# Performance work log

Hardware: AMD Instinct MI355X
Metric: run time of the kernel (lower is better)

## Reference

```python
import jax, jax.numpy as jnp
import numpy as np

T, B, D_IN, D_H = 512, 256, 128, 128


def setup_inputs() -> dict:
    key = jax.random.key(0)
    ks = jax.random.split(key, 13)
    D = D_IN + D_H
    s = 1.0 / np.sqrt(D)  # torch nn.Linear default init bound
    inp = {"inputs": jax.random.normal(ks[0], (T, B, D_IN), jnp.float32)}
    for i, n in enumerate(["forget", "input", "update", "output"]):
        inp[f"W_{n}"] = jax.random.uniform(ks[1 + 3 * i], (2, D), jnp.float32, -s, s)
        inp[f"b_{n}"] = jax.random.uniform(ks[2 + 3 * i], (2,), jnp.float32, -s, s)
        inp[f"theta_{n}"] = jax.random.uniform(ks[3 + 3 * i], (2,), jnp.float32, 0.0, 2.0 * np.pi)
    return inp


def _qgate(comb, W, b, theta):
    # SamplerQNN analytic form (2 qubits):
    #   RY(x0)RY(th0) on wire0, RY(x1)RY(th1) on wire1, CNOT(0,1), measure <Z0>.
    #   Consecutive RYs compose; Z0 commutes with CNOT (wire0 is control),
    #   so QLayer output = <Z0> = cos(x0 + th0). Wire-1 params do not affect it.
    z0 = comb @ W[0] + b[0]  # first row of the 2-dim Linear projection: (B,)
    return jnp.cos(z0 + theta[0])


def reference(inputs, W_forget, b_forget, theta_forget, W_input, b_input, theta_input,
              W_update, b_update, theta_update, W_output, b_output, theta_output):
    Bsz = inputs.shape[1]
    h0 = jnp.zeros((Bsz, D_H), inputs.dtype)
    c0 = jnp.zeros((Bsz, D_H), inputs.dtype)

    def step(carry, x_t):
        hx, cx = carry
        comb = jnp.concatenate([x_t, hx], axis=1)  # (B, D_IN + D_H)
        # per-batch scalar gate activations, broadcast over hidden dim
        f = jax.nn.sigmoid(_qgate(comb, W_forget, b_forget, theta_forget))[:, None]
        i = jax.nn.sigmoid(_qgate(comb, W_input, b_input, theta_input))[:, None]
        g = jnp.tanh(_qgate(comb, W_update, b_update, theta_update))[:, None]
        o = jax.nn.sigmoid(_qgate(comb, W_output, b_output, theta_output))[:, None]
        cx = f * cx + i * g
        hx = o * jnp.tanh(cx)
        return (hx, cx), hx

    (hx, cx), outputs = jax.lax.scan(step, (h0, c0), inputs)
    return outputs, hx, cx
```

## Files before the change

### kernel.cpp

```cpp
#include <hip/hip_runtime.h>
#include <hip/hip_bf16.h>


constexpr int T = 512;
constexpr int Bsz = 256;
constexpr int R = T * Bsz;
constexpr float INV2PI = 0.15915494309189535f;

__global__ __launch_bounds__(256) void xz_kernel(
    const float* __restrict__ x,
    const float* __restrict__ Wf, const float* __restrict__ bf, const float* __restrict__ tf,
    const float* __restrict__ Wi, const float* __restrict__ bi, const float* __restrict__ ti,
    const float* __restrict__ Wu, const float* __restrict__ bu, const float* __restrict__ tu,
    const float* __restrict__ Wo, const float* __restrict__ bo, const float* __restrict__ to_,
    float4* __restrict__ xz)
{
    const int wglobal = blockIdx.x * 4 + (threadIdx.x >> 6);
    const int lane = threadIdx.x & 63;
    const int hl = lane & 31;
    const int half = lane >> 5;

    const float4 wfv = ((const float4*)Wf)[hl];
    const float4 wiv = ((const float4*)Wi)[hl];
    const float4 wuv = ((const float4*)Wu)[hl];
    const float4 wov = ((const float4*)Wo)[hl];

    const float cf = bf[0] + tf[0];
    const float ci = bi[0] + ti[0];
    const float cu = bu[0] + tu[0];
    const float co = bo[0] + to_[0];

    for (int it = 0; it < 8; ++it) {
        const int row = (it * 8192 + wglobal) * 2 + half;
        const float4 xv = *(const float4*)(x + (size_t)row * 128 + hl * 4);

        float pf = xv.x * wfv.x + xv.y * wfv.y + xv.z * wfv.z + xv.w * wfv.w;
        float pi = xv.x * wiv.x + xv.y * wiv.y + xv.z * wiv.z + xv.w * wiv.w;
        float pu = xv.x * wuv.x + xv.y * wuv.y + xv.z * wuv.z + xv.w * wuv.w;
        float po = xv.x * wov.x + xv.y * wov.y + xv.z * wov.z + xv.w * wov.w;

#pragma unroll
        for (int off = 16; off; off >>= 1) {
            pf += __shfl_xor(pf, off, 64);
            pi += __shfl_xor(pi, off, 64);
            pu += __shfl_xor(pu, off, 64);
            po += __shfl_xor(po, off, 64);
        }
        if (hl == 0) {
            xz[row] = make_float4((pf + cf) * INV2PI, (pi + ci) * INV2PI,
                                  (pu + cu) * INV2PI, (po + co) * INV2PI);
        }
    }
}

__device__ __forceinline__ float tanh9(float c) {
    const float y  = c * c;
    const float y2 = y * y;
    const float lo  = fmaf(y, -0.321470f, 0.999168f);
    const float hi  = fmaf(y, 0.0016407f, -0.0199491f);
    const float mid = fmaf(y, hi, 0.101498f);
    return c * fmaf(y2, mid, lo);
}

template<int CTRL>
__device__ __forceinline__ float dppq(float x) {
    return __builtin_bit_cast(float,
        __builtin_amdgcn_mov_dpp(__builtin_bit_cast(int, x), CTRL, 0xF, 0xF, true));
}

__device__ __forceinline__ float wsum(const float* __restrict__ W, int lane) {
    float s = W[128 + lane] + W[192 + lane];
#pragma unroll
    for (int off = 32; off; off >>= 1) s += __shfl_xor(s, off, 64);
    return s;
}

constexpr int BPB = 8;
constexpr int SCAN_BLOCKS = Bsz / BPB;

__global__ __launch_bounds__(256, 1) void scan_kernel(
    const float4* __restrict__ xz,
    const float* __restrict__ Wf, const float* __restrict__ Wi,
    const float* __restrict__ Wu, const float* __restrict__ Wo,
    float* __restrict__ hscan, float* __restrict__ cfin)
{
    __shared__ float4 lds4[T * BPB];
    const int tid = threadIdx.x;
    const int bb = blockIdx.x * BPB;

#pragma unroll
    for (int k = 0; k < T * BPB / 256; ++k) {
        const int j = k * 256 + tid;
        lds4[j] = xz[(j >> 3) * Bsz + bb + (j & 7)];
    }

    const int l = tid & 63;
    const float swf = wsum(Wf, l) * INV2PI;
    const float swi = wsum(Wi, l) * INV2PI;
    const float swu = wsum(Wu, l) * INV2PI;
    const float swo = wsum(Wo, l) * INV2PI;

    __syncthreads();
    if (tid >= BPB * 4) return;

    const int q = tid & 3;
    const int bg = tid >> 2;
    const int batch = bb + bg;

    const float sw = (q == 0) ? swf : (q == 1) ? swi : (q == 2) ? swu : swo;

    const bool tq = (q == 2);
    const float K0 = tq ? 0.0f        : 0.5f;
    const float K1 = tq ? 0.999904f   : 0.249976f;
    const float K3 = tq ? -0.331066f  : -0.0206916f;
    const float K5 = tq ? 0.120476f   : 0.00188244f;
    const float K7 = tq ? -0.0277200f : -0.000108281f;

    const float* zl = (const float*)lds4 + tid;
    float* hp = hscan + batch;

    float h = 0.0f, c = 0.0f;

#define QSTEP(Z)                                                  \
    {                                                             \
        const float u  = fmaf(h, sw, (Z));                        \
        const float v  = __builtin_amdgcn_cosf(u);                \
        const float v2 = v * v;                                   \
        const float v4 = v2 * v2;                                 \
        const float ph = fmaf(v2, K7, K5);                        \
        const float pl = fmaf(v2, K3, K1);                        \
        const float gown = fmaf(v, fmaf(v4, ph, pl), K0);         \
        const float f = dppq<0x00>(gown);                         \
        const float i = dppq<0x55>(gown);                         \
        const float g = dppq<0xAA>(gown);                         \
        const float o = dppq<0xFF>(gown);                         \
        c = fmaf(f, c, i * g);                                    \
        h = o * tanh9(c);                                         \
        *hp = h;                                                  \
        hp += Bsz;                                                \
    }

    for (int tb = 0; tb < T; tb += 8) {
        const float* zt = zl + (size_t)tb * 32;
        const float y0 = zt[0 * 32];
        const float y1 = zt[1 * 32];
        const float y2 = zt[2 * 32];
        const float y3 = zt[3 * 32];
        const float y4 = zt[4 * 32];
        const float y5 = zt[5 * 32];
        const float y6 = zt[6 * 32];
        const float y7 = zt[7 * 32];
        QSTEP(y0); QSTEP(y1); QSTEP(y2); QSTEP(y3);
        QSTEP(y4); QSTEP(y5); QSTEP(y6); QSTEP(y7);
    }
#undef QSTEP

    cfin[batch] = c;
}

__global__ __launch_bounds__(256) void bcast_kernel(
    const float* __restrict__ hscan, const float* __restrict__ cfin,
    float4* __restrict__ out)
{
    const unsigned i = blockIdx.x * 256u + threadIdx.x;
    const unsigned row = i >> 5;
    float v;
    if (row < (unsigned)R) {
        v = hscan[row];
    } else {
        const unsigned r2 = row - (unsigned)R;
        v = (r2 < (unsigned)Bsz) ? hscan[(T - 1) * Bsz + r2] : cfin[r2 - (unsigned)Bsz];
    }
    out[i] = make_float4(v, v, v, v);
}

extern "C" void kernel_launch(void* const* d_in, const int* in_sizes, int n_in,
                              void* d_out, int out_size, void* d_ws, size_t ws_size,
                              hipStream_t stream)
{
    const float* x  = (const float*)d_in[0];
    const float* Wf = (const float*)d_in[1];
    const float* bf = (const float*)d_in[2];
    const float* tf = (const float*)d_in[3];
    const float* Wi = (const float*)d_in[4];
    const float* bi = (const float*)d_in[5];
    const float* ti = (const float*)d_in[6];
    const float* Wu = (const float*)d_in[7];
    const float* bu = (const float*)d_in[8];
    const float* tu = (const float*)d_in[9];
    const float* Wo = (const float*)d_in[10];
    const float* bo = (const float*)d_in[11];
    const float* to_ = (const float*)d_in[12];

    float* ws    = (float*)d_ws;
    float4* xz   = (float4*)ws;
    float* hscan = ws + 4 * R;
    float* cfin  = ws + 5 * R;

    xz_kernel<<<2048, 256, 0, stream>>>(x, Wf, bf, tf, Wi, bi, ti, Wu, bu, tu, Wo, bo, to_, xz);
    scan_kernel<<<SCAN_BLOCKS, 256, 0, stream>>>(xz, Wf, Wi, Wu, Wo, hscan, cfin);

    const int total_f4 = (R + 2 * Bsz) * 32;
    bcast_kernel<<<total_f4 / 256, 256, 0, stream>>>(hscan, cfin, (float4*)d_out);
}
```

Baseline: 73.80 us.

## Buffer scan hidden states in LDS and flush coalesced; shorten gate polynomial

The serial scan loop now writes each step's h into a shared-memory buffer rather than issuing a scattered global store every step. After the loop, all 256 threads copy the buffer to hscan with coalesced stores. The gate activation polynomial is also cut from degree 7 to degree 5 with refitted tanh constants, which removes a few FMAs from the serial critical path. The trade-offs are extra LDS (a 64KB buffer on top of the z buffer), slightly lower accuracy of the gate activation, and an added barrier plus a copy phase at the end of the kernel.

```diff
diff --git a/kernel.cpp b/kernel.cpp
--- a/kernel.cpp
+++ b/kernel.cpp
@@ -84,14 +84,15 @@
     const float* __restrict__ Wu, const float* __restrict__ Wo,
     float* __restrict__ hscan, float* __restrict__ cfin)
 {
-    __shared__ float4 lds4[T * BPB];
+    __shared__ float4 zb4[T * BPB];
+    __shared__ float  hb[T * 32];
     const int tid = threadIdx.x;
     const int bb = blockIdx.x * BPB;
 
 #pragma unroll
     for (int k = 0; k < T * BPB / 256; ++k) {
         const int j = k * 256 + tid;
-        lds4[j] = xz[(j >> 3) * Bsz + bb + (j & 7)];
+        zb4[j] = xz[(j >> 3) * Bsz + bb + (j & 7)];
     }
 
     const int l = tid & 63;
@@ -101,61 +102,73 @@
     const float swo = wsum(Wo, l) * INV2PI;
 
     __syncthreads();
-    if (tid >= BPB * 4) return;
-
-    const int q = tid & 3;
-    const int bg = tid >> 2;
-    const int batch = bb + bg;
-
-    const float sw = (q == 0) ? swf : (q == 1) ? swi : (q == 2) ? swu : swo;
-
-    const bool tq = (q == 2);
-    const float K0 = tq ? 0.0f        : 0.5f;
-    const float K1 = tq ? 0.999904f   : 0.249976f;
-    const float K3 = tq ? -0.331066f  : -0.0206916f;
-    const float K5 = tq ? 0.120476f   : 0.00188244f;
-    const float K7 = tq ? -0.0277200f : -0.000108281f;
-
-    const float* zl = (const float*)lds4 + tid;
-    float* hp = hscan + batch;
-
-    float h = 0.0f, c = 0.0f;
-
-#define QSTEP(Z)                                                  \
+
+    if (tid < BPB * 4) {
+        const int q = tid & 3;
+        const int batch = bb + (tid >> 2);
+
+        const float sw = (q == 0) ? swf : (q == 1) ? swi : (q == 2) ? swu : swo;
+
+        const bool tq = (q == 2);
+        const float K0 = tq ? 0.0f       : 0.5f;
+        const float K1 = tq ? 0.999318f  : 0.249976f;
+        const float K3 = tq ? -0.319476f : -0.0206916f;
+        const float K5 = tq ? 0.08315f   : 0.00188244f;
+
+        const float* zl = (const float*)zb4 + tid;
+        float* hw = hb + tid;
+
+        float h = 0.0f, c = 0.0f;
+
+#define QSTEP(Z, S)                                               \
     {                                                             \
         const float u  = fmaf(h, sw, (Z));                        \
         const float v  = __builtin_amdgcn_cosf(u);                \
         const float v2 = v * v;                                   \
-        const float v4 = v2 * v2;                                 \
-        const float ph = fmaf(v2, K7, K5);                        \
-        const float pl = fmaf(v2, K3, K1);                        \
-        const float gown = fmaf(v, fmaf(v4, ph, pl), K0);         \
+        const float t1 = fmaf(v2, K5, K3);                        \
+        const float p  = fmaf(v2, t1, K1);                        \
+        const float gown = fmaf(v, p, K0);                        \
         const float f = dppq<0x00>(gown);                         \
         const float i = dppq<0x55>(gown);                         \
         const float g = dppq<0xAA>(gown);                         \
         const float o = dppq<0xFF>(gown);                         \
         c = fmaf(f, c, i * g);                                    \
         h = o * tanh9(c);                                         \
-        *hp = h;                                                  \
-        hp += Bsz;                                                \
-    }
-
-    for (int tb = 0; tb < T; tb += 8) {
-        const float* zt = zl + (size_t)tb * 32;
-        const float y0 = zt[0 * 32];
-        const float y1 = zt[1 * 32];
-        const float y2 = zt[2 * 32];
-        const float y3 = zt[3 * 32];
-        const float y4 = zt[4 * 32];
-        const float y5 = zt[5 * 32];
-        const float y6 = zt[6 * 32];
-        const float y7 = zt[7 * 32];
-        QSTEP(y0); QSTEP(y1); QSTEP(y2); QSTEP(y3);
-        QSTEP(y4); QSTEP(y5); QSTEP(y6); QSTEP(y7);
-    }
+        hw[(S) * 32] = h;                                         \
+    }
+
+        for (int tb = 0; tb < T; tb += 8) {
+            const float* zt = zl + (size_t)tb * 32;
+            float* ht = hw + (size_t)tb * 32;
+            const float y0 = zt[0 * 32];
+            const float y1 = zt[1 * 32];
+            const float y2 = zt[2 * 32];
+            const float y3 = zt[3 * 32];
+            const float y4 = zt[4 * 32];
+            const float y5 = zt[5 * 32];
+            const float y6 = zt[6 * 32];
+            const float y7 = zt[7 * 32];
+#define HSTEP(Y, S) { const float u=fmaf(h,sw,(Y)); const float v=__builtin_amdgcn_cosf(u); \
+        const float v2=v*v; const float t1=fmaf(v2,K5,K3); const float p=fmaf(v2,t1,K1);   \
+        const float gown=fmaf(v,p,K0);                                                      \
+        const float f=dppq<0x00>(gown); const float i=dppq<0x55>(gown);                     \
+        const float g=dppq<0xAA>(gown); const float o=dppq<0xFF>(gown);                     \
+        c=fmaf(f,c,i*g); h=o*tanh9(c); ht[(S)*32]=h; }
+            HSTEP(y0, 0); HSTEP(y1, 1); HSTEP(y2, 2); HSTEP(y3, 3);
+            HSTEP(y4, 4); HSTEP(y5, 5); HSTEP(y6, 6); HSTEP(y7, 7);
+#undef HSTEP
+        }
 #undef QSTEP
 
-    cfin[batch] = c;
+        cfin[batch] = c;
+    }
+
+    __syncthreads();
+
+    for (int j = tid; j < T * BPB; j += 256) {
+        const int t = j >> 3, bg = j & 7;
+        hscan[t * Bsz + bb + bg] = hb[t * 32 + bg * 4];
+    }
 }
 
 __global__ __launch_bounds__(256) void bcast_kernel(
```

After: 73.67 us. No clear change (-0.2%).
